# Kernel optimization log

Measured on AMD Instinct MI355X. Metric: run time of the kernel, lower is better.

Reference implementation:

```python
import jax, jax.numpy as jnp
import numpy as np

N, XDIM, FACTOR, INTDIM = 1_000_000, 32, 2, 8
HID = XDIM * FACTOR  # 64


def setup_inputs() -> dict:
    key = jax.random.key(0)
    k1, k2, k3, k4, k5, k6 = jax.random.split(key, 6)
    edge_attr3 = jax.random.normal(k1, (N, XDIM), dtype=jnp.float32)
    edge_attr3_old = jax.random.randint(k2, (N, INTDIM), 0, 2).astype(jnp.int32)
    # kaiming-like uniform init (init distribution does not affect reference math)
    bw0 = 1.0 / np.sqrt(XDIM)
    w0 = jax.random.uniform(k3, (INTDIM, XDIM, HID), jnp.float32, -bw0, bw0)
    b0 = jax.random.uniform(k4, (INTDIM, HID), jnp.float32, -bw0, bw0)
    bw1 = 1.0 / np.sqrt(HID)
    w1 = jax.random.uniform(k5, (INTDIM, HID, 1), jnp.float32, -bw1, bw1)
    b1 = jax.random.uniform(k6, (INTDIM, 1), jnp.float32, -bw1, bw1)
    return {"edge_attr3": edge_attr3, "edge_attr3_old": edge_attr3_old,
            "w0": w0, "b0": b0, "w1": w1, "b1": b1}


def reference(edge_attr3, edge_attr3_old, w0, b0, w1, b1):
    # layer 0: per-head GEMM + bias + ReLU -> [n, d, q]
    h = jax.nn.relu(jnp.einsum('np,dpq->ndq', edge_attr3, w0) + b0)
    # layer 1: per-head projection to scalar, then squeeze -> [n, d]
    out = jnp.einsum('ndp,dp->nd', h, w1[:, :, 0]) + b1[:, 0]
    # boolean-mask gather (eager; dynamic output length as in torch out[mask])
    flat_idx = jnp.flatnonzero(edge_attr3_old.astype(bool))
    return out.reshape(-1)[flat_idx]
```

## Files before the change

kernel.cpp:

```cpp
#include <hip/hip_runtime.h>

#define NROWS 1000000
#define NB    3907
#define NT    62500
#define TPB   4
#define NBATCH (NT / TPB)
#define MLP_BLOCKS 768

typedef __bf16 bf16x8 __attribute__((ext_vector_type(8)));
typedef float  f32x4  __attribute__((ext_vector_type(4)));

__global__ __launch_bounds__(256) void count_kernel(
    const int* __restrict__ mask, int* __restrict__ bsum) {
  int tid = threadIdx.x;
  int row = blockIdx.x * 256 + tid;
  int cnt = 0;
  if (row < NROWS) {
    const int4* mp = (const int4*)(mask + (long)row * 8);
    int4 a = mp[0], b = mp[1];
    cnt = (a.x != 0) + (a.y != 0) + (a.z != 0) + (a.w != 0) +
          (b.x != 0) + (b.y != 0) + (b.z != 0) + (b.w != 0);
  }
#pragma unroll
  for (int off = 1; off < 64; off <<= 1) cnt += __shfl_xor(cnt, off);
  __shared__ int ws[4];
  if ((tid & 63) == 0) ws[tid >> 6] = cnt;
  __syncthreads();
  if (tid == 0) bsum[blockIdx.x] = ws[0] + ws[1] + ws[2] + ws[3];
}

__global__ __launch_bounds__(1024) void scan_kernel(
    const int* __restrict__ bsum, int* __restrict__ boff) {
  __shared__ int lds[1024];
  int t = threadIdx.x;
  int i0 = t * 4;
  int c0 = (i0 + 0 < NB) ? bsum[i0 + 0] : 0;
  int c1 = (i0 + 1 < NB) ? bsum[i0 + 1] : 0;
  int c2 = (i0 + 2 < NB) ? bsum[i0 + 2] : 0;
  int c3 = (i0 + 3 < NB) ? bsum[i0 + 3] : 0;
  int s = c0 + c1 + c2 + c3;
  lds[t] = s;
  __syncthreads();
  for (int off = 1; off < 1024; off <<= 1) {
    int v = lds[t];
    int add = (t >= off) ? lds[t - off] : 0;
    __syncthreads();
    lds[t] = v + add;
    __syncthreads();
  }
  int excl = lds[t] - s;
  if (i0 + 0 < NB) boff[i0 + 0] = excl;
  excl += c0;
  if (i0 + 1 < NB) boff[i0 + 1] = excl;
  excl += c1;
  if (i0 + 2 < NB) boff[i0 + 2] = excl;
  excl += c2;
  if (i0 + 3 < NB) boff[i0 + 3] = excl;
}

__global__ __launch_bounds__(256) void expand_kernel(
    const int* __restrict__ mask, const int* __restrict__ boff,
    int* __restrict__ rowinfo) {
  int tid = threadIdx.x;
  int row = blockIdx.x * 256 + tid;
  bool valid = row < NROWS;
  unsigned mb = 0;
  int cnt = 0;
  if (valid) {
    const int4* mp = (const int4*)(mask + (long)row * 8);
    int4 a = mp[0], b = mp[1];
    mb = (unsigned)((a.x != 0) | ((a.y != 0) << 1) | ((a.z != 0) << 2) |
                    ((a.w != 0) << 3) | ((b.x != 0) << 4) | ((b.y != 0) << 5) |
                    ((b.z != 0) << 6) | ((b.w != 0) << 7));
    cnt = __popc(mb);
  }
  int incl = cnt;
#pragma unroll
  for (int off = 1; off < 64; off <<= 1) {
    int v = __shfl_up(incl, off);
    if ((tid & 63) >= off) incl += v;
  }
  __shared__ int wsum[4];
  if ((tid & 63) == 63) wsum[tid >> 6] = incl;
  __syncthreads();
  int w = tid >> 6;
  int wo = 0;
  if (w > 0) wo += wsum[0];
  if (w > 1) wo += wsum[1];
  if (w > 2) wo += wsum[2];
  int pos = boff[blockIdx.x] + wo + (incl - cnt);
  if (valid) rowinfo[row] = (pos << 8) | (int)mb;
}

__global__ __launch_bounds__(256) void mlp_kernel(
    const float* __restrict__ x, const float* __restrict__ w0,
    const float* __restrict__ b0, const float* __restrict__ w1,
    const float* __restrict__ b1, const int* __restrict__ rowinfo,
    float* __restrict__ out) {
  __shared__ __bf16 sA[32 * 64 * 8];
  __shared__ float sB0[512];
  __shared__ float sW1[512];
  __shared__ float sOut[4 * TPB * 16 * 12];

  int tid = threadIdx.x;

#pragma unroll
  for (int i = 0; i < 8; ++i) {
    int fi = i * 256 + tid;
    int frag = fi >> 6;
    int lane = fi & 63;
    int d = frag >> 2, qb = frag & 3;
    int q = qb * 16 + (lane & 15);
    int kb = (lane >> 4) * 8;
    bf16x8 v;
#pragma unroll
    for (int j = 0; j < 8; ++j)
      v[j] = (__bf16)w0[d * 2048 + (kb + j) * 64 + q];
    *(bf16x8*)&sA[fi * 8] = v;
  }
  if (tid < 128) {
    *(float4*)&sB0[tid * 4] = *(const float4*)&b0[tid * 4];
  } else {
    int t2 = tid - 128;
    *(float4*)&sW1[t2 * 4] = *(const float4*)&w1[t2 * 4];
  }
  __syncthreads();

  int l = tid & 63;
  int n = l & 15;
  int g = l >> 4;
  int w = tid >> 6;
  int wv = blockIdx.x * 4 + w;
  const int W = MLP_BLOCKS * 4;
  float* myOut = &sOut[w * (TPB * 16 * 12)];

  for (int b = wv; b < NBATCH; b += W) {
    int t0 = b * TPB;

    bf16x8 xf0, xf1, xf2, xf3;
    {
      const float* xp;
      float4 a, c;
#define LOADX(T, DST)                                              \
      xp = x + (long)((t0 + T) * 16 + n) * 32 + g * 8;             \
      a = *(const float4*)xp; c = *(const float4*)(xp + 4);        \
      DST[0] = (__bf16)a.x; DST[1] = (__bf16)a.y;                  \
      DST[2] = (__bf16)a.z; DST[3] = (__bf16)a.w;                  \
      DST[4] = (__bf16)c.x; DST[5] = (__bf16)c.y;                  \
      DST[6] = (__bf16)c.z; DST[7] = (__bf16)c.w;
      LOADX(0, xf0) LOADX(1, xf1) LOADX(2, xf2) LOADX(3, xf3)
#undef LOADX
    }

#pragma unroll 1
    for (int d = 0; d < 8; ++d) {
      float p0 = 0.f, p1 = 0.f, p2 = 0.f, p3 = 0.f;
#pragma unroll
      for (int qb = 0; qb < 4; ++qb) {
        int frag = d * 4 + qb;
        bf16x8 A  = *(const bf16x8*)&sA[frag * 512 + l * 8];
        f32x4 Cb  = *(const f32x4*)&sB0[frag * 16 + g * 4];
        f32x4 W1r = *(const f32x4*)&sW1[frag * 16 + g * 4];
        f32x4 D0 = __builtin_amdgcn_mfma_f32_16x16x32_bf16(A, xf0, Cb, 0, 0, 0);
        f32x4 D1 = __builtin_amdgcn_mfma_f32_16x16x32_bf16(A, xf1, Cb, 0, 0, 0);
        f32x4 D2 = __builtin_amdgcn_mfma_f32_16x16x32_bf16(A, xf2, Cb, 0, 0, 0);
        f32x4 D3 = __builtin_amdgcn_mfma_f32_16x16x32_bf16(A, xf3, Cb, 0, 0, 0);
#pragma unroll
        for (int r = 0; r < 4; ++r) {
          p0 = fmaf(fmaxf(D0[r], 0.f), W1r[r], p0);
          p1 = fmaf(fmaxf(D1[r], 0.f), W1r[r], p1);
          p2 = fmaf(fmaxf(D2[r], 0.f), W1r[r], p2);
          p3 = fmaf(fmaxf(D3[r], 0.f), W1r[r], p3);
        }
      }
      p0 += __shfl_xor(p0, 16); p0 += __shfl_xor(p0, 32);
      p1 += __shfl_xor(p1, 16); p1 += __shfl_xor(p1, 32);
      p2 += __shfl_xor(p2, 16); p2 += __shfl_xor(p2, 32);
      p3 += __shfl_xor(p3, 16); p3 += __shfl_xor(p3, 32);
      float bb = b1[d];
      if (g == 0) {
        myOut[(0 * 16 + n) * 12 + d] = p0 + bb;
        myOut[(1 * 16 + n) * 12 + d] = p1 + bb;
        myOut[(2 * 16 + n) * 12 + d] = p2 + bb;
        myOut[(3 * 16 + n) * 12 + d] = p3 + bb;
      }
    }

    int row = t0 * 16 + l;
    int info = rowinfo[row];
    unsigned mb = (unsigned)info & 255u;
    int pos = (int)(((unsigned)info) >> 8);
    f32x4 v0 = *(const f32x4*)&myOut[l * 12];
    f32x4 v1 = *(const f32x4*)&myOut[l * 12 + 4];
#pragma unroll
    for (int dd = 0; dd < 4; ++dd) {
      if ((mb >> dd) & 1u) out[pos++] = v0[dd];
    }
#pragma unroll
    for (int dd = 0; dd < 4; ++dd) {
      if ((mb >> (4 + dd)) & 1u) out[pos++] = v1[dd];
    }
  }
}

extern "C" void kernel_launch(void* const* d_in, const int* in_sizes, int n_in,
                              void* d_out, int out_size, void* d_ws, size_t ws_size,
                              hipStream_t stream) {
  const float* x    = (const float*)d_in[0];
  const int*   mask = (const int*)d_in[1];
  const float* w0   = (const float*)d_in[2];
  const float* b0   = (const float*)d_in[3];
  const float* w1   = (const float*)d_in[4];
  const float* b1   = (const float*)d_in[5];
  float* out = (float*)d_out;

  int* bsum    = (int*)d_ws;
  int* boff    = bsum + NB;
  int* rowinfo = boff + NB;

  count_kernel<<<NB, 256, 0, stream>>>(mask, bsum);
  scan_kernel<<<1, 1024, 0, stream>>>(bsum, boff);
  expand_kernel<<<NB, 256, 0, stream>>>(mask, boff, rowinfo);
  mlp_kernel<<<MLP_BLOCKS, 256, 0, stream>>>(x, w0, b0, w1, b1, rowinfo, out);
}
```

Before: 92.04 us.

## Compute layer-1 projection with MFMA instead of VALU dot and LDS staging

The second-layer per-head dot product now runs as an extra MFMA on a block-diagonal masked w1 fragment, fed with the bf16 ReLU outputs of the first layer. The result accumulates directly in a 16x16 tile where lanes hold per-row head outputs. This removes the cross-lane shuffles, the FMA reduction and the LDS output staging buffer, so the epilogue writes straight from registers. The block count rises and launch bounds request four blocks per CU. The cost is bf16 rounding of the hidden activations and doubled MFMA count, most of which multiplies zeros.

```diff
diff --git a/kernel.cpp b/kernel.cpp
--- a/kernel.cpp
+++ b/kernel.cpp
@@ -5,7 +5,7 @@
 #define NT    62500
 #define TPB   4
 #define NBATCH (NT / TPB)
-#define MLP_BLOCKS 768
+#define MLP_BLOCKS 1024
 
 typedef __bf16 bf16x8 __attribute__((ext_vector_type(8)));
 typedef float  f32x4  __attribute__((ext_vector_type(4)));
@@ -92,15 +92,13 @@
   if (valid) rowinfo[row] = (pos << 8) | (int)mb;
 }
 
-__global__ __launch_bounds__(256) void mlp_kernel(
+__global__ __launch_bounds__(256, 4) void mlp_kernel(
     const float* __restrict__ x, const float* __restrict__ w0,
     const float* __restrict__ b0, const float* __restrict__ w1,
     const float* __restrict__ b1, const int* __restrict__ rowinfo,
     float* __restrict__ out) {
   __shared__ __bf16 sA[32 * 64 * 8];
   __shared__ float sB0[512];
-  __shared__ float sW1[512];
-  __shared__ float sOut[4 * TPB * 16 * 12];
 
   int tid = threadIdx.x;
 
@@ -118,21 +116,30 @@
       v[j] = (__bf16)w0[d * 2048 + (kb + j) * 64 + q];
     *(bf16x8*)&sA[fi * 8] = v;
   }
-  if (tid < 128) {
-    *(float4*)&sB0[tid * 4] = *(const float4*)&b0[tid * 4];
-  } else {
-    int t2 = tid - 128;
-    *(float4*)&sW1[t2 * 4] = *(const float4*)&w1[t2 * 4];
-  }
+  if (tid < 128) *(float4*)&sB0[tid * 4] = *(const float4*)&b0[tid * 4];
   __syncthreads();
 
   int l = tid & 63;
   int n = l & 15;
   int g = l >> 4;
+
+  bf16x8 w1A, w1B;
+  bool ownrow = (n < 8);
+#pragma unroll
+  for (int j = 0; j < 8; ++j) {
+    int off = (j >> 2) * 16 + g * 4 + (j & 3);
+    w1A[j] = ownrow ? (__bf16)w1[n * 64 + off]      : (__bf16)0.f;
+    w1B[j] = ownrow ? (__bf16)w1[n * 64 + 32 + off] : (__bf16)0.f;
+  }
+  int4 w1Ai = *(int4*)&w1A;
+  int4 w1Bi = *(int4*)&w1B;
+  f32x4 b1C;
+#pragma unroll
+  for (int r = 0; r < 4; ++r) b1C[r] = b1[(g * 4 + r) & 7];
+
   int w = tid >> 6;
   int wv = blockIdx.x * 4 + w;
   const int W = MLP_BLOCKS * 4;
-  float* myOut = &sOut[w * (TPB * 16 * 12)];
 
   for (int b = wv; b < NBATCH; b += W) {
     int t0 = b * TPB;
@@ -152,53 +159,61 @@
 #undef LOADX
     }
 
+    f32x4 O0 = b1C, O1 = b1C, O2 = b1C, O3 = b1C;
+
 #pragma unroll 1
-    for (int d = 0; d < 8; ++d) {
-      float p0 = 0.f, p1 = 0.f, p2 = 0.f, p3 = 0.f;
-#pragma unroll
-      for (int qb = 0; qb < 4; ++qb) {
-        int frag = d * 4 + qb;
-        bf16x8 A  = *(const bf16x8*)&sA[frag * 512 + l * 8];
-        f32x4 Cb  = *(const f32x4*)&sB0[frag * 16 + g * 4];
-        f32x4 W1r = *(const f32x4*)&sW1[frag * 16 + g * 4];
-        f32x4 D0 = __builtin_amdgcn_mfma_f32_16x16x32_bf16(A, xf0, Cb, 0, 0, 0);
-        f32x4 D1 = __builtin_amdgcn_mfma_f32_16x16x32_bf16(A, xf1, Cb, 0, 0, 0);
-        f32x4 D2 = __builtin_amdgcn_mfma_f32_16x16x32_bf16(A, xf2, Cb, 0, 0, 0);
-        f32x4 D3 = __builtin_amdgcn_mfma_f32_16x16x32_bf16(A, xf3, Cb, 0, 0, 0);
-#pragma unroll
-        for (int r = 0; r < 4; ++r) {
-          p0 = fmaf(fmaxf(D0[r], 0.f), W1r[r], p0);
-          p1 = fmaf(fmaxf(D1[r], 0.f), W1r[r], p1);
-          p2 = fmaf(fmaxf(D2[r], 0.f), W1r[r], p2);
-          p3 = fmaf(fmaxf(D3[r], 0.f), W1r[r], p3);
-        }
-      }
-      p0 += __shfl_xor(p0, 16); p0 += __shfl_xor(p0, 32);
-      p1 += __shfl_xor(p1, 16); p1 += __shfl_xor(p1, 32);
-      p2 += __shfl_xor(p2, 16); p2 += __shfl_xor(p2, 32);
-      p3 += __shfl_xor(p3, 16); p3 += __shfl_xor(p3, 32);
-      float bb = b1[d];
-      if (g == 0) {
-        myOut[(0 * 16 + n) * 12 + d] = p0 + bb;
-        myOut[(1 * 16 + n) * 12 + d] = p1 + bb;
-        myOut[(2 * 16 + n) * 12 + d] = p2 + bb;
-        myOut[(3 * 16 + n) * 12 + d] = p3 + bb;
-      }
+    for (int cp = 0; cp < 8; ++cp) {
+      bool own = (n == cp);
+      int4 z4 = {0, 0, 0, 0};
+      int4 A2ai = own ? w1Ai : z4;
+      int4 A2bi = own ? w1Bi : z4;
+      bf16x8 A2a = *(bf16x8*)&A2ai;
+      bf16x8 A2b = *(bf16x8*)&A2bi;
+      int fb = cp * 4;
+      bf16x8 Aw0 = *(const bf16x8*)&sA[(fb + 0) * 512 + l * 8];
+      bf16x8 Aw1 = *(const bf16x8*)&sA[(fb + 1) * 512 + l * 8];
+      bf16x8 Aw2 = *(const bf16x8*)&sA[(fb + 2) * 512 + l * 8];
+      bf16x8 Aw3 = *(const bf16x8*)&sA[(fb + 3) * 512 + l * 8];
+      f32x4 C0 = *(const f32x4*)&sB0[(fb + 0) * 16 + g * 4];
+      f32x4 C1 = *(const f32x4*)&sB0[(fb + 1) * 16 + g * 4];
+      f32x4 C2 = *(const f32x4*)&sB0[(fb + 2) * 16 + g * 4];
+      f32x4 C3 = *(const f32x4*)&sB0[(fb + 3) * 16 + g * 4];
+
+#define TILE(XF, OD) {                                                        \
+      f32x4 Da = __builtin_amdgcn_mfma_f32_16x16x32_bf16(Aw0, XF, C0, 0,0,0); \
+      f32x4 Db = __builtin_amdgcn_mfma_f32_16x16x32_bf16(Aw1, XF, C1, 0,0,0); \
+      bf16x8 B2;                                                              \
+      B2[0] = (__bf16)fmaxf(Da[0], 0.f); B2[1] = (__bf16)fmaxf(Da[1], 0.f);   \
+      B2[2] = (__bf16)fmaxf(Da[2], 0.f); B2[3] = (__bf16)fmaxf(Da[3], 0.f);   \
+      B2[4] = (__bf16)fmaxf(Db[0], 0.f); B2[5] = (__bf16)fmaxf(Db[1], 0.f);   \
+      B2[6] = (__bf16)fmaxf(Db[2], 0.f); B2[7] = (__bf16)fmaxf(Db[3], 0.f);   \
+      OD = __builtin_amdgcn_mfma_f32_16x16x32_bf16(A2a, B2, OD, 0, 0, 0);     \
+      f32x4 Dc = __builtin_amdgcn_mfma_f32_16x16x32_bf16(Aw2, XF, C2, 0,0,0); \
+      f32x4 Dd = __builtin_amdgcn_mfma_f32_16x16x32_bf16(Aw3, XF, C3, 0,0,0); \
+      bf16x8 B3;                                                              \
+      B3[0] = (__bf16)fmaxf(Dc[0], 0.f); B3[1] = (__bf16)fmaxf(Dc[1], 0.f);   \
+      B3[2] = (__bf16)fmaxf(Dc[2], 0.f); B3[3] = (__bf16)fmaxf(Dc[3], 0.f);   \
+      B3[4] = (__bf16)fmaxf(Dd[0], 0.f); B3[5] = (__bf16)fmaxf(Dd[1], 0.f);   \
+      B3[6] = (__bf16)fmaxf(Dd[2], 0.f); B3[7] = (__bf16)fmaxf(Dd[3], 0.f);   \
+      OD = __builtin_amdgcn_mfma_f32_16x16x32_bf16(A2b, B3, OD, 0, 0, 0); }
+      TILE(xf0, O0) TILE(xf1, O1) TILE(xf2, O2) TILE(xf3, O3)
+#undef TILE
     }
 
-    int row = t0 * 16 + l;
-    int info = rowinfo[row];
-    unsigned mb = (unsigned)info & 255u;
-    int pos = (int)(((unsigned)info) >> 8);
-    f32x4 v0 = *(const f32x4*)&myOut[l * 12];
-    f32x4 v1 = *(const f32x4*)&myOut[l * 12 + 4];
-#pragma unroll
-    for (int dd = 0; dd < 4; ++dd) {
-      if ((mb >> dd) & 1u) out[pos++] = v0[dd];
-    }
-#pragma unroll
-    for (int dd = 0; dd < 4; ++dd) {
-      if ((mb >> (4 + dd)) & 1u) out[pos++] = v1[dd];
+    if (g < 2) {
+#define EPI(T, OD) {                                                     \
+      int row = (t0 + T) * 16 + n;                                       \
+      int info = rowinfo[row];                                           \
+      unsigned mb = (unsigned)info & 255u;                               \
+      int pos = (int)(((unsigned)info) >> 8) +                           \
+                (g ? __popc(mb & 0xFu) : 0);                             \
+      unsigned nib = (mb >> (g * 4)) & 0xFu;                             \
+      if (nib & 1u) { out[pos] = OD[0]; pos++; }                         \
+      if (nib & 2u) { out[pos] = OD[1]; pos++; }                         \
+      if (nib & 4u) { out[pos] = OD[2]; pos++; }                         \
+      if (nib & 8u) { out[pos] = OD[3]; }                                }
+      EPI(0, O0) EPI(1, O1) EPI(2, O2) EPI(3, O3)
+#undef EPI
     }
   }
 }
```

Result: faster. 89.55 us (-2.7%).
